# Kernel optimization log

Hardware: AMD Instinct MI355X
Metric: run time of the kernel (lower is better)

The kernel has to match this reference:

```python
import jax, jax.numpy as jnp
import numpy as np

B, T, TAU = 4, 512, 512
D_MODEL = 1024  # in_dim == out_dim (required: pos embedding dim out_dim feeds pos_proj with in_size=in_dim)
H, D = 16, 64
LN_EPS = 1e-5


def rel_shift(x):
    # x: [B, T, L, H] -> Transformer-XL relative shift
    b, t, l, h = x.shape
    x = jnp.pad(x, ((0, 0), (0, 0), (1, 0), (0, 0)))  # pad j-dim front
    x = x.reshape(b, l + 1, t, h)[:, 1:, :, :]
    return x.reshape(b, t, l, h)


def setup_inputs() -> dict:
    key = jax.random.key(0)
    ks = jax.random.split(key, 7)
    s = 0.02
    return {
        "inputs": jax.random.normal(ks[0], (B, T, D_MODEL), jnp.float32),
        "memory": jax.random.normal(ks[1], (B, TAU, D_MODEL), jnp.float32),
        "w_qkv": jax.random.normal(ks[2], (3 * H * D, D_MODEL), jnp.float32) * s,
        "w_pos": jax.random.normal(ks[3], (H * D, D_MODEL), jnp.float32) * s,
        "w_out": jax.random.normal(ks[4], (D_MODEL, H * D), jnp.float32) * s,
        "uvar": jax.random.normal(ks[5], (H, D), jnp.float32) * s,
        "vvar": jax.random.normal(ks[6], (H, D), jnp.float32) * s,
        "ln_gamma": jnp.ones((D_MODEL,), jnp.float32),
        "ln_beta": jnp.zeros((D_MODEL,), jnp.float32),
    }


def reference(inputs, memory, w_qkv, w_pos, w_out, uvar, vvar, ln_gamma, ln_beta):
    b, t, din = inputs.shape
    tau = memory.shape[1]
    L = tau + t
    h, d = uvar.shape

    x = jnp.concatenate([jax.lax.stop_gradient(memory), inputs], axis=1)  # [B,L,Din]
    # input layernorm
    mu = jnp.mean(x, axis=-1, keepdims=True)
    var = jnp.mean((x - mu) ** 2, axis=-1, keepdims=True)
    x = (x - mu) / jnp.sqrt(var + LN_EPS) * ln_gamma + ln_beta

    qkv = x @ w_qkv.T  # [B,L,3HD]
    q, k, v = jnp.split(qkv, 3, axis=-1)
    q = q[:, -t:].reshape(b, t, h, d)
    k = k.reshape(b, L, h, d)
    v = v.reshape(b, L, h, d)

    # sinusoidal relative position embedding, dim = out_dim (= din here)
    inv_freq = 1.0 / (10000.0 ** (jnp.arange(0, din, 2, dtype=jnp.float32) / din))
    pos = jnp.arange(L - 1, -1, -1, dtype=jnp.float32)
    sin_in = pos[:, None] * inv_freq[None, :]                 # [L, din/2]
    phi = jnp.concatenate([jnp.sin(sin_in), jnp.cos(sin_in)], axis=-1)  # [L, din]
    R = (phi @ w_pos.T).reshape(L, h, d)

    score = jnp.einsum('bihd,bjhd->bijh', q + uvar, k)        # content score
    pos_score = jnp.einsum('bihd,jhd->bijh', q + vvar, R)     # position score
    score = (score + rel_shift(pos_score)) / (d ** 0.5)       # [B,T,L,H]

    # causal mask: query i attends to j <= tau + i
    mask = (jnp.arange(L)[None, :] <= (tau + jnp.arange(t))[:, None]).astype(score.dtype)
    mask = mask[None, :, :, None]
    masked = score * mask + 1e30 * (mask - 1.0)
    w = jax.nn.softmax(masked, axis=2)

    out = jnp.einsum('bijh,bjhd->bihd', w, v).reshape(b, t, h * d)
    return out @ w_out.T
```

## Files before the change

kernel.cpp:

```cpp
#include <hip/hip_runtime.h>
#include <math.h>

#define B_   4
#define T_   512
#define TAU_ 512
#define L_   1024
#define DM_  1024
#define H_   16
#define D_   64

typedef short  s16x8 __attribute__((ext_vector_type(8)));
typedef ushort u16x4 __attribute__((ext_vector_type(4)));
typedef float  f32x4 __attribute__((ext_vector_type(4)));

__device__ __forceinline__ ushort f2bf(float x) {
  uint u = __float_as_uint(x);
  u += 0x7fffu + ((u >> 16) & 1u);
  return (ushort)(u >> 16);
}
__device__ __forceinline__ float bf2f(ushort u) {
  return __uint_as_float(((uint)u) << 16);
}
__device__ __forceinline__ int sw64(int row, int col) {
  return row * 64 + (col ^ ((row & 7) << 3));
}

__global__ __launch_bounds__(256) void ln_concat_kernel(
    const float* __restrict__ inp, const float* __restrict__ mem,
    const float* __restrict__ gamma, const float* __restrict__ beta,
    ushort* __restrict__ xn) {
  int row = blockIdx.x;
  int b = row >> 10, l = row & 1023;
  const float* src = (l < TAU_)
      ? mem + ((size_t)b * TAU_ + l) * DM_
      : inp + ((size_t)b * T_ + (l - TAU_)) * DM_;
  int t = threadIdx.x;
  float4 v = *(const float4*)(src + t * 4);
  float s  = v.x + v.y + v.z + v.w;
  float s2 = v.x * v.x + v.y * v.y + v.z * v.z + v.w * v.w;
#pragma unroll
  for (int off = 32; off > 0; off >>= 1) {
    s  += __shfl_down(s, off);
    s2 += __shfl_down(s2, off);
  }
  __shared__ float red[8];
  __shared__ float stat[2];
  int wid = t >> 6;
  if ((t & 63) == 0) { red[wid * 2] = s; red[wid * 2 + 1] = s2; }
  __syncthreads();
  if (t == 0) {
    float ts  = red[0] + red[2] + red[4] + red[6];
    float ts2 = red[1] + red[3] + red[5] + red[7];
    float mu  = ts * (1.0f / DM_);
    float var = ts2 * (1.0f / DM_) - mu * mu;
    stat[0] = mu;
    stat[1] = 1.0f / sqrtf(var + 1e-5f);
  }
  __syncthreads();
  float mu = stat[0], rstd = stat[1];
  float4 g  = *(const float4*)(gamma + t * 4);
  float4 be = *(const float4*)(beta  + t * 4);
  u16x4 o;
  o[0] = f2bf((v.x - mu) * rstd * g.x + be.x);
  o[1] = f2bf((v.y - mu) * rstd * g.y + be.y);
  o[2] = f2bf((v.z - mu) * rstd * g.z + be.z);
  o[3] = f2bf((v.w - mu) * rstd * g.w + be.w);
  *(u16x4*)(xn + (size_t)row * DM_ + t * 4) = o;
}

__global__ __launch_bounds__(256) void phi_kernel(ushort* __restrict__ phi) {
  int idx = blockIdx.x * 256 + threadIdx.x;
  int m = idx >> 10, c = idx & 1023;
  float p = (float)(1023 - m);
  int cc = (c < 512) ? c : c - 512;
  float invf = __expf(-((float)(2 * cc) * (1.0f / 1024.0f)) * 9.210340371976184f);
  float a = p * invf;
  phi[idx] = f2bf((c < 512) ? sinf(a) : cosf(a));
}

__global__ __launch_bounds__(256) void cast_bf16_kernel(
    const float* __restrict__ in, ushort* __restrict__ out, int n4) {
  int i = blockIdx.x * 256 + threadIdx.x;
  if (i >= n4) return;
  float4 v = *(const float4*)(in + (size_t)i * 4);
  u16x4 o = { f2bf(v.x), f2bf(v.y), f2bf(v.z), f2bf(v.w) };
  *(u16x4*)(out + (size_t)i * 4) = o;
}

template <typename CT>
__global__ __launch_bounds__(256) void gemm_nt_bf16(
    const ushort* __restrict__ A, const ushort* __restrict__ B,
    CT* __restrict__ C, int M, int N, int K) {
  __shared__ __attribute__((aligned(16))) ushort As[128 * 32];
  __shared__ __attribute__((aligned(16))) ushort Bs[128 * 32];
  int t = threadIdx.x;
  int w = t >> 6, lane = t & 63, g = lane >> 4, low = lane & 15;
  int wr = w >> 1, wc = w & 1;
  int m0 = blockIdx.y * 128, n0 = blockIdx.x * 128;
  f32x4 acc[4][4] = {};

  for (int kt = 0; kt < K; kt += 32) {
    __syncthreads();
#pragma unroll
    for (int q = 0; q < 2; ++q) {
      int f = t + q * 256;
      int row = f >> 2;
      int gslot = (f & 3) ^ ((row >> 1) & 3);
      const ushort* ga = A + (size_t)(m0 + row) * K + kt + gslot * 8;
      const ushort* gb = B + (size_t)(n0 + row) * K + kt + gslot * 8;
      __builtin_amdgcn_global_load_lds(
          (const __attribute__((address_space(1))) void*)ga,
          (__attribute__((address_space(3))) void*)&As[(q * 256 + w * 64) * 8],
          16, 0, 0);
      __builtin_amdgcn_global_load_lds(
          (const __attribute__((address_space(1))) void*)gb,
          (__attribute__((address_space(3))) void*)&Bs[(q * 256 + w * 64) * 8],
          16, 0, 0);
    }
    __syncthreads();

    s16x8 af[4], bfr[4];
#pragma unroll
    for (int mi = 0; mi < 4; ++mi) {
      int row = wr * 64 + mi * 16 + low;
      af[mi] = *(const s16x8*)&As[row * 32 + ((g ^ ((row >> 1) & 3)) * 8)];
    }
#pragma unroll
    for (int ni = 0; ni < 4; ++ni) {
      int col = wc * 64 + ni * 16 + low;
      bfr[ni] = *(const s16x8*)&Bs[col * 32 + ((g ^ ((col >> 1) & 3)) * 8)];
    }
#pragma unroll
    for (int mi = 0; mi < 4; ++mi)
#pragma unroll
      for (int ni = 0; ni < 4; ++ni)
        acc[mi][ni] = __builtin_amdgcn_mfma_f32_16x16x32_bf16(
            af[mi], bfr[ni], acc[mi][ni], 0, 0, 0);
  }
#pragma unroll
  for (int mi = 0; mi < 4; ++mi)
#pragma unroll
    for (int ni = 0; ni < 4; ++ni)
#pragma unroll
      for (int r = 0; r < 4; ++r) {
        int m = m0 + wr * 64 + mi * 16 + 4 * g + r;
        int n = n0 + wc * 64 + ni * 16 + low;
        if constexpr (sizeof(CT) == 2)
          C[(size_t)m * N + n] = f2bf(acc[mi][ni][r]);
        else
          C[(size_t)m * N + n] = acc[mi][ni][r];
      }
}

__global__ __launch_bounds__(256) void vtrans_kernel(
    const ushort* __restrict__ qkv, ushort* __restrict__ vtg) {
  __shared__ ushort vs[64 * 65];
  int bid = blockIdx.x;
  int lt = bid & 15;
  int h  = (bid >> 4) & 15;
  int b  = bid >> 8;
  int l0 = lt * 64;
  int t = threadIdx.x;
#pragma unroll
  for (int q = 0; q < 2; ++q) {
    int c = t + q * 256;
    int row = c >> 3, sl = c & 7;
    s16x8 v = *(const s16x8*)(qkv +
        (size_t)(b * L_ + l0 + row) * 3072 + 2048 + h * 64 + sl * 8);
#pragma unroll
    for (int e = 0; e < 8; ++e) vs[row * 65 + sl * 8 + e] = (ushort)v[e];
  }
  __syncthreads();
#pragma unroll
  for (int q = 0; q < 2; ++q) {
    int c = t + q * 256;
    int d = c >> 3, sl = c & 7;
    s16x8 o;
#pragma unroll
    for (int e = 0; e < 8; ++e) o[e] = (short)vs[(sl * 8 + e) * 65 + d];
    *(s16x8*)(vtg + (size_t)((b * 16 + h) * 64 + d) * 1024 + l0 + sl * 8) = o;
  }
}

__global__ __launch_bounds__(256) void attn_mfma_kernel(
    const ushort* __restrict__ qkv, const ushort* __restrict__ Rm,
    const ushort* __restrict__ vtg,
    const float* __restrict__ uvar, const float* __restrict__ vvar,
    ushort* __restrict__ attn) {
  __shared__ __attribute__((aligned(16))) ushort Ks[2][64 * 64];
  __shared__ __attribute__((aligned(16))) ushort Vt[2][64 * 64];
  __shared__ __attribute__((aligned(16))) ushort Rs[2][128 * 64];
  __shared__ __attribute__((aligned(16))) ushort Pp[4][16 * 64];

  int t   = threadIdx.x;
  int w   = t >> 6;
  int lw  = t & 63;
  int g   = lw >> 4;
  int low = lw & 15;

  int bid = blockIdx.x;
  int bi  = bid & 7;
  int h   = (bid >> 3) & 15;
  int b   = bid >> 7;
  int i0  = bi * 64;
  int lb_w = 48 - 16 * w;

  auto stage = [&](int buf, int tl) {
    int j0s = tl * 64;
#pragma unroll
    for (int q = 0; q < 2; ++q) {
      int c = t + q * 256;
      int row = c >> 3;
      int sl = (c & 7) ^ (row & 7);
      const ushort* srck = qkv + (size_t)(b * L_ + j0s + row) * 3072 +
                           1024 + h * 64 + sl * 8;
      __builtin_amdgcn_global_load_lds(
          (const __attribute__((address_space(1))) void*)srck,
          (__attribute__((address_space(3))) void*)&Ks[buf][(q * 256 + w * 64) * 8],
          16, 0, 0);
      const ushort* srcv = vtg + (size_t)((b * 16 + h) * 64 + row) * 1024 +
                           j0s + sl * 8;
      __builtin_amdgcn_global_load_lds(
          (const __attribute__((address_space(1))) void*)srcv,
          (__attribute__((address_space(3))) void*)&Vt[buf][(q * 256 + w * 64) * 8],
          16, 0, 0);
    }
    int mb = j0s + 448 - i0;
#pragma unroll
    for (int q = 0; q < 4; ++q) {
      int c = t + q * 256;
      int row = c >> 3;
      int m = mb + row; m = (m > 1023) ? 1023 : m;
      int sl = (c & 7) ^ (row & 7);
      const ushort* srcr = Rm + (size_t)m * 1024 + h * 64 + sl * 8;
      __builtin_amdgcn_global_load_lds(
          (const __attribute__((address_space(1))) void*)srcr,
          (__attribute__((address_space(3))) void*)&Rs[buf][(q * 256 + w * 64) * 8],
          16, 0, 0);
    }
  };

  int iq = i0 + 16 * w + low;
  s16x8 qu[2], qv[2];
  {
    const ushort* qrow = qkv + (size_t)(b * L_ + TAU_ + iq) * 3072 + h * 64;
    const float* ur = uvar + h * 64;
    const float* vr = vvar + h * 64;
#pragma unroll
    for (int kc = 0; kc < 2; ++kc) {
      int dbase = kc * 32 + 8 * g;
#pragma unroll
      for (int e = 0; e < 8; ++e) {
        float q = bf2f(qrow[dbase + e]);
        qu[kc][e] = (short)f2bf(q + ur[dbase + e]);
        qv[kc][e] = (short)f2bf(q + vr[dbase + e]);
      }
    }
  }

  f32x4 O[4] = {};
  float mreg[4] = {-INFINITY, -INFINITY, -INFINITY, -INFINITY};
  float lreg[4] = {0.f, 0.f, 0.f, 0.f};

  int ntiles = 9 + bi;
  stage(0, 0);
  __syncthreads();
  int cur = 0;
  for (int tile = 0; tile < ntiles; ++tile) {
    int j0 = tile * 64;
    if (tile + 1 < ntiles) stage(cur ^ 1, tile + 1);

    f32x4 s[4] = {};
#pragma unroll
    for (int jt = 0; jt < 4; ++jt) {
#pragma unroll
      for (int kc = 0; kc < 2; ++kc) {
        s16x8 kb = *(const s16x8*)&Ks[cur][sw64(jt * 16 + low, kc * 32 + 8 * g)];
        s[jt] = __builtin_amdgcn_mfma_f32_16x16x32_bf16(qu[kc], kb, s[jt], 0, 0, 0);
      }
    }
    f32x4 p[5] = {};
#pragma unroll
    for (int mt = 0; mt < 5; ++mt) {
#pragma unroll
      for (int kc = 0; kc < 2; ++kc) {
        s16x8 rb = *(const s16x8*)&Rs[cur][sw64(lb_w + mt * 16 + low, kc * 32 + 8 * g)];
        p[mt] = __builtin_amdgcn_mfma_f32_16x16x32_bf16(qv[kc], rb, p[mt], 0, 0, 0);
      }
    }
#pragma unroll
    for (int r = 0; r < 4; ++r) {
      int iL = 4 * g + r;
      int src = g * 16 + ((low + 15 - iL) & 15);
      float sh0 = __shfl(p[0][r], src);
      float sh1 = __shfl(p[1][r], src);
      float sh2 = __shfl(p[2][r], src);
      float sh3 = __shfl(p[3][r], src);
      float sh4 = __shfl(p[4][r], src);
      bool lo = (low <= iL);
      float po0 = lo ? sh0 : sh1;
      float po1 = lo ? sh1 : sh2;
      float po2 = lo ? sh2 : sh3;
      float po3 = lo ? sh3 : sh4;
      int lim = TAU_ + i0 + 16 * w + iL;
      s[0][r] = (j0 + 0 * 16 + low <= lim) ? (s[0][r] + po0) * 0.125f : -1e30f;
      s[1][r] = (j0 + 1 * 16 + low <= lim) ? (s[1][r] + po1) * 0.125f : -1e30f;
      s[2][r] = (j0 + 2 * 16 + low <= lim) ? (s[2][r] + po2) * 0.125f : -1e30f;
      s[3][r] = (j0 + 3 * 16 + low <= lim) ? (s[3][r] + po3) * 0.125f : -1e30f;
    }
#pragma unroll
    for (int r = 0; r < 4; ++r) {
      float mx = fmaxf(fmaxf(s[0][r], s[1][r]), fmaxf(s[2][r], s[3][r]));
      mx = fmaxf(mx, __shfl_xor(mx, 1));
      mx = fmaxf(mx, __shfl_xor(mx, 2));
      mx = fmaxf(mx, __shfl_xor(mx, 4));
      mx = fmaxf(mx, __shfl_xor(mx, 8));
      float mn = fmaxf(mreg[r], mx);
      float alpha = __expf(mreg[r] - mn);
      mreg[r] = mn;
      float sum = 0.f;
#pragma unroll
      for (int jt = 0; jt < 4; ++jt) {
        float pe = __expf(s[jt][r] - mn);
        s[jt][r] = pe;
        sum += pe;
      }
      sum += __shfl_xor(sum, 1);
      sum += __shfl_xor(sum, 2);
      sum += __shfl_xor(sum, 4);
      sum += __shfl_xor(sum, 8);
      lreg[r] = lreg[r] * alpha + sum;
      O[0][r] *= alpha; O[1][r] *= alpha; O[2][r] *= alpha; O[3][r] *= alpha;
    }
#pragma unroll
    for (int jt = 0; jt < 4; ++jt)
#pragma unroll
      for (int r = 0; r < 4; ++r)
        Pp[w][sw64(4 * g + r, jt * 16 + low)] = f2bf(s[jt][r]);
    asm volatile("s_waitcnt lgkmcnt(0)" ::: "memory");
    s16x8 pa0 = *(const s16x8*)&Pp[w][sw64(low, 8 * g)];
    s16x8 pa1 = *(const s16x8*)&Pp[w][sw64(low, 32 + 8 * g)];
#pragma unroll
    for (int dt = 0; dt < 4; ++dt) {
      s16x8 v0 = *(const s16x8*)&Vt[cur][sw64(dt * 16 + low, 8 * g)];
      s16x8 v1 = *(const s16x8*)&Vt[cur][sw64(dt * 16 + low, 32 + 8 * g)];
      O[dt] = __builtin_amdgcn_mfma_f32_16x16x32_bf16(pa0, v0, O[dt], 0, 0, 0);
      O[dt] = __builtin_amdgcn_mfma_f32_16x16x32_bf16(pa1, v1, O[dt], 0, 0, 0);
    }
    __syncthreads();
    cur ^= 1;
  }
  float inv[4];
#pragma unroll
  for (int r = 0; r < 4; ++r) inv[r] = 1.0f / lreg[r];
#pragma unroll
  for (int dt = 0; dt < 4; ++dt)
#pragma unroll
    for (int r = 0; r < 4; ++r)
      attn[((size_t)(b * T_ + i0 + 16 * w + 4 * g + r)) * 1024 +
           h * 64 + dt * 16 + low] = f2bf(O[dt][r] * inv[r]);
}

extern "C" void kernel_launch(void* const* d_in, const int* in_sizes, int n_in,
                              void* d_out, int out_size, void* d_ws, size_t ws_size,
                              hipStream_t stream) {
  const float* inputs = (const float*)d_in[0];
  const float* memory = (const float*)d_in[1];
  const float* w_qkv  = (const float*)d_in[2];
  const float* w_pos  = (const float*)d_in[3];
  const float* w_out  = (const float*)d_in[4];
  const float* uvar   = (const float*)d_in[5];
  const float* vvar   = (const float*)d_in[6];
  const float* gamma  = (const float*)d_in[7];
  const float* beta   = (const float*)d_in[8];
  float* out = (float*)d_out;

  ushort* qkvB = (ushort*)d_ws;
  ushort* xnb  = qkvB + (size_t)4096 * 3072;
  ushort* phib = xnb  + (size_t)4096 * 1024;
  ushort* RmB  = phib + (size_t)1024 * 1024;
  ushort* wqb  = RmB  + (size_t)1024 * 1024;
  ushort* wpb  = wqb  + (size_t)3072 * 1024;
  ushort* wob  = wpb  + (size_t)1024 * 1024;
  ushort* vtg  = wob  + (size_t)1024 * 1024;
  ushort* attnb = xnb;

  ln_concat_kernel<<<B_ * L_, 256, 0, stream>>>(inputs, memory, gamma, beta, xnb);
  phi_kernel<<<(L_ * DM_) / 256, 256, 0, stream>>>(phib);
  cast_bf16_kernel<<<(3072 * 1024 / 4 + 255) / 256, 256, 0, stream>>>(w_qkv, wqb, 3072 * 1024 / 4);
  cast_bf16_kernel<<<(1024 * 1024 / 4 + 255) / 256, 256, 0, stream>>>(w_pos, wpb, 1024 * 1024 / 4);
  cast_bf16_kernel<<<(1024 * 1024 / 4 + 255) / 256, 256, 0, stream>>>(w_out, wob, 1024 * 1024 / 4);

  gemm_nt_bf16<ushort><<<dim3(3072 / 128, 4096 / 128), 256, 0, stream>>>(
      xnb, wqb, qkvB, 4096, 3072, 1024);
  gemm_nt_bf16<ushort><<<dim3(1024 / 128, 1024 / 128), 256, 0, stream>>>(
      phib, wpb, RmB, 1024, 1024, 1024);
  vtrans_kernel<<<B_ * H_ * 16, 256, 0, stream>>>(qkvB, vtg);
  attn_mfma_kernel<<<dim3(B_ * H_ * 8), 256, 0, stream>>>(qkvB, RmB, vtg, uvar, vvar, attnb);
  gemm_nt_bf16<float><<<dim3(1024 / 128, 2048 / 128), 256, 0, stream>>>(
      attnb, wob, out, 2048, 1024, 1024);
}
```

Baseline: 237.8 us.

## Merge prep kernels and GEMMs, add setprio, exp2 softmax, causal balancing

The five elementwise prep kernels (layernorm, phi, three weight casts) become one launch, and the QKV and R projections share a single GEMM launch. This cuts launch overhead and lets the small R GEMM fill idle CUs. The attention kernel now raises wave priority around MFMA blocks and reverses the query-block order on odd heads to balance causal work. It skips mask checks on fully valid tiles and folds the softmax scale into log2 so it can use exp2. Risks are small rounding changes and uneven block shapes inside the merged launches.

```diff
diff --git a/kernel.cpp b/kernel.cpp
--- a/kernel.cpp
+++ b/kernel.cpp
@@ -13,6 +13,8 @@
 typedef ushort u16x4 __attribute__((ext_vector_type(4)));
 typedef float  f32x4 __attribute__((ext_vector_type(4)));
 
+#define SC_LOG2 0.18033688011f
+
 __device__ __forceinline__ ushort f2bf(float x) {
   uint u = __float_as_uint(x);
   u += 0x7fffu + ((u >> 16) & 1u);
@@ -25,78 +27,82 @@
   return row * 64 + (col ^ ((row & 7) << 3));
 }
 
-__global__ __launch_bounds__(256) void ln_concat_kernel(
+__global__ __launch_bounds__(256) void prep_kernel(
     const float* __restrict__ inp, const float* __restrict__ mem,
     const float* __restrict__ gamma, const float* __restrict__ beta,
-    ushort* __restrict__ xn) {
-  int row = blockIdx.x;
-  int b = row >> 10, l = row & 1023;
-  const float* src = (l < TAU_)
-      ? mem + ((size_t)b * TAU_ + l) * DM_
-      : inp + ((size_t)b * T_ + (l - TAU_)) * DM_;
+    ushort* __restrict__ xn, ushort* __restrict__ phi,
+    const float* __restrict__ wq, ushort* __restrict__ wqb,
+    const float* __restrict__ wp, ushort* __restrict__ wpb,
+    const float* __restrict__ wo, ushort* __restrict__ wob) {
+  int blk = blockIdx.x;
   int t = threadIdx.x;
-  float4 v = *(const float4*)(src + t * 4);
-  float s  = v.x + v.y + v.z + v.w;
-  float s2 = v.x * v.x + v.y * v.y + v.z * v.z + v.w * v.w;
-#pragma unroll
-  for (int off = 32; off > 0; off >>= 1) {
-    s  += __shfl_down(s, off);
-    s2 += __shfl_down(s2, off);
-  }
-  __shared__ float red[8];
-  __shared__ float stat[2];
-  int wid = t >> 6;
-  if ((t & 63) == 0) { red[wid * 2] = s; red[wid * 2 + 1] = s2; }
-  __syncthreads();
-  if (t == 0) {
-    float ts  = red[0] + red[2] + red[4] + red[6];
-    float ts2 = red[1] + red[3] + red[5] + red[7];
-    float mu  = ts * (1.0f / DM_);
-    float var = ts2 * (1.0f / DM_) - mu * mu;
-    stat[0] = mu;
-    stat[1] = 1.0f / sqrtf(var + 1e-5f);
-  }
-  __syncthreads();
-  float mu = stat[0], rstd = stat[1];
-  float4 g  = *(const float4*)(gamma + t * 4);
-  float4 be = *(const float4*)(beta  + t * 4);
-  u16x4 o;
-  o[0] = f2bf((v.x - mu) * rstd * g.x + be.x);
-  o[1] = f2bf((v.y - mu) * rstd * g.y + be.y);
-  o[2] = f2bf((v.z - mu) * rstd * g.z + be.z);
-  o[3] = f2bf((v.w - mu) * rstd * g.w + be.w);
-  *(u16x4*)(xn + (size_t)row * DM_ + t * 4) = o;
-}
-
-__global__ __launch_bounds__(256) void phi_kernel(ushort* __restrict__ phi) {
-  int idx = blockIdx.x * 256 + threadIdx.x;
-  int m = idx >> 10, c = idx & 1023;
-  float p = (float)(1023 - m);
-  int cc = (c < 512) ? c : c - 512;
-  float invf = __expf(-((float)(2 * cc) * (1.0f / 1024.0f)) * 9.210340371976184f);
-  float a = p * invf;
-  phi[idx] = f2bf((c < 512) ? sinf(a) : cosf(a));
-}
-
-__global__ __launch_bounds__(256) void cast_bf16_kernel(
-    const float* __restrict__ in, ushort* __restrict__ out, int n4) {
-  int i = blockIdx.x * 256 + threadIdx.x;
-  if (i >= n4) return;
-  float4 v = *(const float4*)(in + (size_t)i * 4);
-  u16x4 o = { f2bf(v.x), f2bf(v.y), f2bf(v.z), f2bf(v.w) };
-  *(u16x4*)(out + (size_t)i * 4) = o;
+  if (blk < 4096) {
+    int row = blk;
+    int b = row >> 10, l = row & 1023;
+    const float* src = (l < TAU_)
+        ? mem + ((size_t)b * TAU_ + l) * DM_
+        : inp + ((size_t)b * T_ + (l - TAU_)) * DM_;
+    float4 v = *(const float4*)(src + t * 4);
+    float s  = v.x + v.y + v.z + v.w;
+    float s2 = v.x * v.x + v.y * v.y + v.z * v.z + v.w * v.w;
+#pragma unroll
+    for (int off = 32; off > 0; off >>= 1) {
+      s  += __shfl_down(s, off);
+      s2 += __shfl_down(s2, off);
+    }
+    __shared__ float red[8];
+    __shared__ float stat[2];
+    int wid = t >> 6;
+    if ((t & 63) == 0) { red[wid * 2] = s; red[wid * 2 + 1] = s2; }
+    __syncthreads();
+    if (t == 0) {
+      float ts  = red[0] + red[2] + red[4] + red[6];
+      float ts2 = red[1] + red[3] + red[5] + red[7];
+      float mu  = ts * (1.0f / DM_);
+      float var = ts2 * (1.0f / DM_) - mu * mu;
+      stat[0] = mu;
+      stat[1] = 1.0f / sqrtf(var + 1e-5f);
+    }
+    __syncthreads();
+    float mu = stat[0], rstd = stat[1];
+    float4 g  = *(const float4*)(gamma + t * 4);
+    float4 be = *(const float4*)(beta  + t * 4);
+    u16x4 o;
+    o[0] = f2bf((v.x - mu) * rstd * g.x + be.x);
+    o[1] = f2bf((v.y - mu) * rstd * g.y + be.y);
+    o[2] = f2bf((v.z - mu) * rstd * g.z + be.z);
+    o[3] = f2bf((v.w - mu) * rstd * g.w + be.w);
+    *(u16x4*)(xn + (size_t)row * DM_ + t * 4) = o;
+  } else if (blk < 8192) {
+    int idx = (blk - 4096) * 256 + t;
+    int m = idx >> 10, c = idx & 1023;
+    float p = (float)(1023 - m);
+    int cc = (c < 512) ? c : c - 512;
+    float invf = __expf(-((float)(2 * cc) * (1.0f / 1024.0f)) * 9.210340371976184f);
+    float a = p * invf;
+    phi[idx] = f2bf((c < 512) ? sinf(a) : cosf(a));
+  } else {
+    int i = (blk - 8192) * 256 + t;
+    const float* src; ushort* dst; int off;
+    if (i < 786432)       { src = wq; dst = wqb; off = i; }
+    else if (i < 1048576) { src = wp; dst = wpb; off = i - 786432; }
+    else                  { src = wo; dst = wob; off = i - 1048576; }
+    float4 v = *(const float4*)(src + (size_t)off * 4);
+    u16x4 o = { f2bf(v.x), f2bf(v.y), f2bf(v.z), f2bf(v.w) };
+    *(u16x4*)(dst + (size_t)off * 4) = o;
+  }
 }
 
 template <typename CT>
-__global__ __launch_bounds__(256) void gemm_nt_bf16(
+__device__ __forceinline__ void gemm_nt_body(
     const ushort* __restrict__ A, const ushort* __restrict__ B,
-    CT* __restrict__ C, int M, int N, int K) {
+    CT* __restrict__ C, int M, int N, int K, int bx, int by) {
   __shared__ __attribute__((aligned(16))) ushort As[128 * 32];
   __shared__ __attribute__((aligned(16))) ushort Bs[128 * 32];
   int t = threadIdx.x;
   int w = t >> 6, lane = t & 63, g = lane >> 4, low = lane & 15;
   int wr = w >> 1, wc = w & 1;
-  int m0 = blockIdx.y * 128, n0 = blockIdx.x * 128;
+  int m0 = by * 128, n0 = bx * 128;
   f32x4 acc[4][4] = {};
 
   for (int kt = 0; kt < K; kt += 32) {
@@ -130,12 +136,14 @@
       int col = wc * 64 + ni * 16 + low;
       bfr[ni] = *(const s16x8*)&Bs[col * 32 + ((g ^ ((col >> 1) & 3)) * 8)];
     }
+    __builtin_amdgcn_s_setprio(1);
 #pragma unroll
     for (int mi = 0; mi < 4; ++mi)
 #pragma unroll
       for (int ni = 0; ni < 4; ++ni)
         acc[mi][ni] = __builtin_amdgcn_mfma_f32_16x16x32_bf16(
             af[mi], bfr[ni], acc[mi][ni], 0, 0, 0);
+    __builtin_amdgcn_s_setprio(0);
   }
 #pragma unroll
   for (int mi = 0; mi < 4; ++mi)
@@ -150,6 +158,27 @@
         else
           C[(size_t)m * N + n] = acc[mi][ni][r];
       }
+}
+
+__global__ __launch_bounds__(256) void qkv_r_gemm(
+    const ushort* __restrict__ xnb, const ushort* __restrict__ wqb,
+    ushort* __restrict__ qkvB,
+    const ushort* __restrict__ phib, const ushort* __restrict__ wpb,
+    ushort* __restrict__ RmB) {
+  int id = blockIdx.x;
+  if (id < 768)
+    gemm_nt_body<ushort>(xnb, wqb, qkvB, 4096, 3072, 1024, id % 24, id / 24);
+  else {
+    id -= 768;
+    gemm_nt_body<ushort>(phib, wpb, RmB, 1024, 1024, 1024, id % 8, id / 8);
+  }
+}
+
+__global__ __launch_bounds__(256) void out_gemm(
+    const ushort* __restrict__ attnb, const ushort* __restrict__ wob,
+    float* __restrict__ out) {
+  gemm_nt_body<float>(attnb, wob, out, 2048, 1024, 1024,
+                      blockIdx.x % 8, blockIdx.x / 8);
 }
 
 __global__ __launch_bounds__(256) void vtrans_kernel(
@@ -199,9 +228,10 @@
   int low = lw & 15;
 
   int bid = blockIdx.x;
-  int bi  = bid & 7;
+  int bi_r = bid & 7;
   int h   = (bid >> 3) & 15;
   int b   = bid >> 7;
+  int bi  = (h & 1) ? (7 - bi_r) : bi_r;
   int i0  = bi * 64;
   int lb_w = 48 - 16 * w;
 
@@ -271,6 +301,8 @@
     if (tile + 1 < ntiles) stage(cur ^ 1, tile + 1);
 
     f32x4 s[4] = {};
+    f32x4 p[5] = {};
+    __builtin_amdgcn_s_setprio(1);
 #pragma unroll
     for (int jt = 0; jt < 4; ++jt) {
 #pragma unroll
@@ -279,7 +311,6 @@
         s[jt] = __builtin_amdgcn_mfma_f32_16x16x32_bf16(qu[kc], kb, s[jt], 0, 0, 0);
       }
     }
-    f32x4 p[5] = {};
 #pragma unroll
     for (int mt = 0; mt < 5; ++mt) {
 #pragma unroll
@@ -288,6 +319,9 @@
         p[mt] = __builtin_amdgcn_mfma_f32_16x16x32_bf16(qv[kc], rb, p[mt], 0, 0, 0);
       }
     }
+    __builtin_amdgcn_s_setprio(0);
+
+    bool fullvalid = (j0 + 63 <= TAU_ + i0 + 16 * w);
 #pragma unroll
     for (int r = 0; r < 4; ++r) {
       int iL = 4 * g + r;
@@ -302,11 +336,18 @@
       float po1 = lo ? sh1 : sh2;
       float po2 = lo ? sh2 : sh3;
       float po3 = lo ? sh3 : sh4;
-      int lim = TAU_ + i0 + 16 * w + iL;
-      s[0][r] = (j0 + 0 * 16 + low <= lim) ? (s[0][r] + po0) * 0.125f : -1e30f;
-      s[1][r] = (j0 + 1 * 16 + low <= lim) ? (s[1][r] + po1) * 0.125f : -1e30f;
-      s[2][r] = (j0 + 2 * 16 + low <= lim) ? (s[2][r] + po2) * 0.125f : -1e30f;
-      s[3][r] = (j0 + 3 * 16 + low <= lim) ? (s[3][r] + po3) * 0.125f : -1e30f;
+      if (fullvalid) {
+        s[0][r] = (s[0][r] + po0) * SC_LOG2;
+        s[1][r] = (s[1][r] + po1) * SC_LOG2;
+        s[2][r] = (s[2][r] + po2) * SC_LOG2;
+        s[3][r] = (s[3][r] + po3) * SC_LOG2;
+      } else {
+        int lim = TAU_ + i0 + 16 * w + iL;
+        s[0][r] = (j0 +  0 + low <= lim) ? (s[0][r] + po0) * SC_LOG2 : -1e30f;
+        s[1][r] = (j0 + 16 + low <= lim) ? (s[1][r] + po1) * SC_LOG2 : -1e30f;
+        s[2][r] = (j0 + 32 + low <= lim) ? (s[2][r] + po2) * SC_LOG2 : -1e30f;
+        s[3][r] = (j0 + 48 + low <= lim) ? (s[3][r] + po3) * SC_LOG2 : -1e30f;
+      }
     }
 #pragma unroll
     for (int r = 0; r < 4; ++r) {
@@ -316,12 +357,12 @@
       mx = fmaxf(mx, __shfl_xor(mx, 4));
       mx = fmaxf(mx, __shfl_xor(mx, 8));
       float mn = fmaxf(mreg[r], mx);
-      float alpha = __expf(mreg[r] - mn);
+      float alpha = exp2f(mreg[r] - mn);
       mreg[r] = mn;
       float sum = 0.f;
 #pragma unroll
       for (int jt = 0; jt < 4; ++jt) {
-        float pe = __expf(s[jt][r] - mn);
+        float pe = exp2f(s[jt][r] - mn);
         s[jt][r] = pe;
         sum += pe;
       }
@@ -340,6 +381,7 @@
     asm volatile("s_waitcnt lgkmcnt(0)" ::: "memory");
     s16x8 pa0 = *(const s16x8*)&Pp[w][sw64(low, 8 * g)];
     s16x8 pa1 = *(const s16x8*)&Pp[w][sw64(low, 32 + 8 * g)];
+    __builtin_amdgcn_s_setprio(1);
 #pragma unroll
     for (int dt = 0; dt < 4; ++dt) {
       s16x8 v0 = *(const s16x8*)&Vt[cur][sw64(dt * 16 + low, 8 * g)];
@@ -347,6 +389,7 @@
       O[dt] = __builtin_amdgcn_mfma_f32_16x16x32_bf16(pa0, v0, O[dt], 0, 0, 0);
       O[dt] = __builtin_amdgcn_mfma_f32_16x16x32_bf16(pa1, v1, O[dt], 0, 0, 0);
     }
+    __builtin_amdgcn_s_setprio(0);
     __syncthreads();
     cur ^= 1;
   }
@@ -385,18 +428,10 @@
   ushort* vtg  = wob  + (size_t)1024 * 1024;
   ushort* attnb = xnb;
 
-  ln_concat_kernel<<<B_ * L_, 256, 0, stream>>>(inputs, memory, gamma, beta, xnb);
-  phi_kernel<<<(L_ * DM_) / 256, 256, 0, stream>>>(phib);
-  cast_bf16_kernel<<<(3072 * 1024 / 4 + 255) / 256, 256, 0, stream>>>(w_qkv, wqb, 3072 * 1024 / 4);
-  cast_bf16_kernel<<<(1024 * 1024 / 4 + 255) / 256, 256, 0, stream>>>(w_pos, wpb, 1024 * 1024 / 4);
-  cast_bf16_kernel<<<(1024 * 1024 / 4 + 255) / 256, 256, 0, stream>>>(w_out, wob, 1024 * 1024 / 4);
-
-  gemm_nt_bf16<ushort><<<dim3(3072 / 128, 4096 / 128), 256, 0, stream>>>(
-      xnb, wqb, qkvB, 4096, 3072, 1024);
-  gemm_nt_bf16<ushort><<<dim3(1024 / 128, 1024 / 128), 256, 0, stream>>>(
-      phib, wpb, RmB, 1024, 1024, 1024);
+  prep_kernel<<<13312, 256, 0, stream>>>(inputs, memory, gamma, beta, xnb,
+                                         phib, w_qkv, wqb, w_pos, wpb, w_out, wob);
+  qkv_r_gemm<<<832, 256, 0, stream>>>(xnb, wqb, qkvB, phib, wpb, RmB);
   vtrans_kernel<<<B_ * H_ * 16, 256, 0, stream>>>(qkvB, vtg);
   attn_mfma_kernel<<<dim3(B_ * H_ * 8), 256, 0, stream>>>(qkvB, RmB, vtg, uvar, vvar, attnb);
-  gemm_nt_bf16<float><<<dim3(1024 / 128, 2048 / 128), 256, 0, stream>>>(
-      attnb, wob, out, 2048, 1024, 1024);
-}
+  out_gemm<<<128, 256, 0, stream>>>(attnb, wob, out);
+}
```

New measurement: 229.4 us. -3.5%, faster.
